# Kernel tuning notes

Measured on AMD Instinct MI355X. Metric: run time of the kernel, lower is better.

The kernel has to match this reference:

```python
import jax, jax.numpy as jnp
import numpy as np

EMBED_DIM = 768
NUM_HEADS = 12
HEAD_DIM = EMBED_DIM // NUM_HEADS


def setup_inputs() -> dict:
    key = jax.random.key(0)
    ks = jax.random.split(key, 9)
    B, N, D = 8, 1024, EMBED_DIM
    s = 1.0 / np.sqrt(D)
    x = jax.random.normal(ks[0], (B, N, D), dtype=jnp.float32)
    Wq = jax.random.normal(ks[1], (D, D), dtype=jnp.float32) * s
    bq = jnp.zeros((D,), dtype=jnp.float32)
    Wk = jax.random.normal(ks[2], (D, D), dtype=jnp.float32) * s
    bk = jnp.zeros((D,), dtype=jnp.float32)
    Wv = jax.random.normal(ks[3], (D, D), dtype=jnp.float32) * s
    bv = jnp.zeros((D,), dtype=jnp.float32)
    Wo = jax.random.normal(ks[4], (D, D), dtype=jnp.float32) * s
    bo = jnp.zeros((D,), dtype=jnp.float32)
    return {"x": x, "Wq": Wq, "bq": bq, "Wk": Wk, "bk": bk,
            "Wv": Wv, "bv": bv, "Wo": Wo, "bo": bo}


def reference(x, Wq, bq, Wk, bk, Wv, bv, Wo, bo):
    B, N, D = x.shape
    H, Hd = NUM_HEADS, HEAD_DIM
    # torch Linear: y = x @ W.T + b
    q = (x @ Wq.T + bq).reshape(B, N, H, Hd).transpose(0, 2, 1, 3)  # [B,H,N,Hd]
    k = (x @ Wk.T + bk).reshape(B, N, H, Hd).transpose(0, 2, 1, 3)
    v = (x @ Wv.T + bv).reshape(B, N, H, Hd).transpose(0, 2, 1, 3)
    # NOTE: original scales by embed_dim**-0.5 (not head_dim)
    scale = jnp.asarray(D, x.dtype) ** -0.5
    scores = jnp.einsum('bhnd,bhmd->bhnm', q, k) * scale  # [B,H,N,N]
    attn = jax.nn.softmax(scores, axis=-1)
    out = jnp.einsum('bhnm,bhmd->bhnd', attn, v)  # dropout: identity in eval
    out = out.transpose(0, 2, 1, 3).reshape(B, N, D)
    return out @ Wo.T + bo
```

## Files before the change

kernel.cpp:

```cpp
#include <hip/hip_runtime.h>
#include <math.h>


typedef __bf16 bf16x8 __attribute__((ext_vector_type(8)));
typedef float  f32x4  __attribute__((ext_vector_type(4)));
typedef unsigned u32x2 __attribute__((ext_vector_type(2)));
typedef unsigned u32x4 __attribute__((ext_vector_type(4)));
typedef unsigned short ushort_t;

__device__ __forceinline__ unsigned short f2bf(float f) {
    unsigned u = __float_as_uint(f);
    u += 0x7fffu + ((u >> 16) & 1u);
    return (unsigned short)(u >> 16);
}
__device__ __forceinline__ unsigned pk16(unsigned short lo, unsigned short hi) {
    return (unsigned)lo | ((unsigned)hi << 16);
}

#define GLL16(g, l)                                                                        \
    __builtin_amdgcn_global_load_lds((const __attribute__((address_space(1))) void*)(g),   \
                                     (__attribute__((address_space(3))) void*)(l), 16, 0, 0)

__global__ __launch_bounds__(256)
void cast_all(const float* __restrict__ x,
              const float* __restrict__ w0, const float* __restrict__ w1,
              const float* __restrict__ w2, const float* __restrict__ w3,
              ushort_t* __restrict__ xb, ushort_t* __restrict__ wb0,
              ushort_t* __restrict__ wb1, ushort_t* __restrict__ wb2,
              ushort_t* __restrict__ wb3)
{
    const int y = blockIdx.y;
    const float* s; ushort_t* d; int n;
    switch (y) {
        case 0:  s = x;  d = xb;  n = 8192 * 768; break;
        case 1:  s = w0; d = wb0; n = 768 * 768;  break;
        case 2:  s = w1; d = wb1; n = 768 * 768;  break;
        case 3:  s = w2; d = wb2; n = 768 * 768;  break;
        default: s = w3; d = wb3; n = 768 * 768;  break;
    }
    const int i = (blockIdx.x * 256 + threadIdx.x) * 8;
    if (i >= n) return;
    const float4 f0 = *(const float4*)(s + i);
    const float4 f1 = *(const float4*)(s + i + 4);
    ushort4 p0, p1;
    p0.x = f2bf(f0.x); p0.y = f2bf(f0.y); p0.z = f2bf(f0.z); p0.w = f2bf(f0.w);
    p1.x = f2bf(f1.x); p1.y = f2bf(f1.y); p1.z = f2bf(f1.z); p1.w = f2bf(f1.w);
    *(ushort4*)(d + i)     = p0;
    *(ushort4*)(d + i + 4) = p1;
}

__device__ __forceinline__ void gemm_core_mfma(
    const ushort_t* __restrict__ A, const ushort_t* __restrict__ W,
    int m0, int n0, ushort_t* smem, f32x4 acc[4][4])
{
    ushort_t* As = smem;
    ushort_t* Ws = smem + 4096;
    const int tid = threadIdx.x;
    const int L   = tid & 63;
    const int wv  = tid >> 6;
    const int wr  = wv >> 1, wc = wv & 1;
    const int c   = L & 15,  g  = L >> 4;

    const int c0 = tid, c1 = tid + 256;
    const int qs = ((tid & 3) ^ ((tid >> 3) & 3)) * 8;
    const ushort_t* a0 = A + (size_t)(m0 + (c0 >> 2)) * 768 + qs;
    const ushort_t* a1 = A + (size_t)(m0 + (c1 >> 2)) * 768 + qs;
    const ushort_t* w0 = W + (size_t)(n0 + (c0 >> 2)) * 768 + qs;
    const ushort_t* w1 = W + (size_t)(n0 + (c1 >> 2)) * 768 + qs;
    const int sg = (g ^ ((c >> 1) & 3)) * 8;

#pragma unroll
    for (int i = 0; i < 4; ++i)
#pragma unroll
        for (int j = 0; j < 4; ++j) acc[i][j] = (f32x4){0.f, 0.f, 0.f, 0.f};

    for (int k0 = 0; k0 < 768; k0 += 32) {
        __syncthreads();
        GLL16(a0 + k0, &As[(size_t)c0 * 8]);
        GLL16(a1 + k0, &As[(size_t)c1 * 8]);
        GLL16(w0 + k0, &Ws[(size_t)c0 * 8]);
        GLL16(w1 + k0, &Ws[(size_t)c1 * 8]);
        __syncthreads();
        bf16x8 af[4], bfr[4];
#pragma unroll
        for (int i = 0; i < 4; ++i)
            af[i] = *(const bf16x8*)&As[(wr * 64 + i * 16 + c) * 32 + sg];
#pragma unroll
        for (int j = 0; j < 4; ++j)
            bfr[j] = *(const bf16x8*)&Ws[(wc * 64 + j * 16 + c) * 32 + sg];
#pragma unroll
        for (int i = 0; i < 4; ++i)
#pragma unroll
            for (int j = 0; j < 4; ++j)
                acc[i][j] = __builtin_amdgcn_mfma_f32_16x16x32_bf16(
                    af[i], bfr[j], acc[i][j], 0, 0, 0);
    }
}

__global__ __launch_bounds__(256, 3)
void gemm_qkv(const ushort_t* __restrict__ xb,
              const ushort_t* __restrict__ wqb, const ushort_t* __restrict__ wkb,
              const ushort_t* __restrict__ wvb,
              const float* __restrict__ bq, const float* __restrict__ bk,
              const float* __restrict__ bv,
              ushort_t* __restrict__ Qh, ushort_t* __restrict__ Kl,
              ushort_t* __restrict__ Vl)
{
    __shared__ ushort_t smem[8192];
    const int z = blockIdx.z;
    const ushort_t* W   = (z == 0) ? wqb : (z == 1) ? wkb : wvb;
    const float*    bia = (z == 0) ? bq  : (z == 1) ? bk  : bv;
    const int m0 = blockIdx.y * 128, n0 = blockIdx.x * 128;
    f32x4 acc[4][4];
    gemm_core_mfma(xb, W, m0, n0, smem, acc);

    const int tid = threadIdx.x, L = tid & 63, wv2 = tid >> 6;
    const int wr = wv2 >> 1, wc = wv2 & 1, c = L & 15, g = L >> 4;
    ushort_t* scr = smem + wv2 * 1280;
    const int h = (n0 + wc * 64) >> 6;
    float bsv[4];
#pragma unroll
    for (int j = 0; j < 4; ++j) bsv[j] = bia[n0 + wc * 64 + j * 16 + c];

    __syncthreads();
#pragma unroll
    for (int i = 0; i < 4; ++i) {
        const int rowg = m0 + wr * 64 + i * 16;
        const int b  = rowg >> 10;
        const int nb = rowg & 1023;
        const int bh = b * 12 + h;
        if (z < 2) {
#pragma unroll
            for (int j = 0; j < 4; ++j)
#pragma unroll
                for (int r = 0; r < 4; ++r)
                    scr[(g * 4 + r) * 72 + j * 16 + c] = f2bf(acc[i][j][r] + bsv[j]);
            if (z == 0) {
                const int row = L >> 2, qp = L & 3;
                const u32x4 v0 = *(const u32x4*)&scr[row * 72 + qp * 16];
                const u32x4 v1 = *(const u32x4*)&scr[row * 72 + qp * 16 + 8];
                ushort_t* dst = Qh + ((size_t)bh * 1024 + nb + row) * 64 + qp * 16;
                *(u32x4*)dst       = v0;
                *(u32x4*)(dst + 8) = v1;
            } else {
                const int n16 = L >> 2, q1 = L & 3;
                const u32x4 va  = *(const u32x4*)&scr[n16 * 72 + q1 * 8];
                const u32x4 vb2 = *(const u32x4*)&scr[n16 * 72 + q1 * 8 + 32];
                ushort_t* base = Kl + (size_t)bh * 65536 + (size_t)(nb >> 4) * 1024;
                *(u32x4*)&base[q1 * 128 + n16 * 8]       = va;
                *(u32x4*)&base[512 + q1 * 128 + n16 * 8] = vb2;
            }
        } else {
#pragma unroll
            for (int j = 0; j < 4; ++j) {
                const unsigned w01 = pk16(f2bf(acc[i][j][0] + bsv[j]),
                                          f2bf(acc[i][j][1] + bsv[j]));
                const unsigned w23 = pk16(f2bf(acc[i][j][2] + bsv[j]),
                                          f2bf(acc[i][j][3] + bsv[j]));
                const int a = (j * 16 + c) * 20 + g * 4;
                *(unsigned*)&scr[a]     = w01;
                *(unsigned*)&scr[a + 2] = w23;
            }
            const u32x2 r0 = *(const u32x2*)&scr[L * 20];
            const u32x2 r1 = *(const u32x2*)&scr[L * 20 + 4];
            const u32x2 r2 = *(const u32x2*)&scr[L * 20 + 8];
            const u32x2 r3 = *(const u32x2*)&scr[L * 20 + 12];
            const int ht = L >> 4, cV = L & 15;
            const int T = nb >> 6, u = (nb >> 5) & 1, gVa = (nb >> 3) & 3;
            ushort_t* vb = Vl + (((size_t)(bh * 4 + ht) * 16 + T) * 2 + u) * 512 + cV * 8;
            *(u32x4*)&vb[gVa * 128]       = (u32x4){r0.x, r0.y, r1.x, r1.y};
            *(u32x4*)&vb[(gVa + 1) * 128] = (u32x4){r2.x, r2.y, r3.x, r3.y};
        }
    }
}

__global__ __launch_bounds__(256, 3)
void gemm_outp(const ushort_t* __restrict__ attnb, const ushort_t* __restrict__ wob,
               const float* __restrict__ bo, float* __restrict__ out)
{
    __shared__ ushort_t smem[8192];
    const int m0 = blockIdx.y * 128, n0 = blockIdx.x * 128;
    f32x4 acc[4][4];
    gemm_core_mfma(attnb, wob, m0, n0, smem, acc);
    const int tid = threadIdx.x, L = tid & 63, wv2 = tid >> 6;
    const int wr = wv2 >> 1, wc = wv2 & 1, c = L & 15, g = L >> 4;
#pragma unroll
    for (int i = 0; i < 4; ++i) {
        const int row = m0 + wr * 64 + i * 16 + g * 4;
#pragma unroll
        for (int j = 0; j < 4; ++j) {
            const int col = n0 + wc * 64 + j * 16 + c;
            const float bsvo = bo[col];
#pragma unroll
            for (int r = 0; r < 4; ++r)
                out[(size_t)(row + r) * 768 + col] = acc[i][j][r] + bsvo;
        }
    }
}

union FlashSmem {
    ushort_t ps[2][2][16 * 68];
    f32x4 comb[2][64 * 5];
};

__global__ __launch_bounds__(128, 3)
void flash_bf16(const ushort_t* __restrict__ Q, const ushort_t* __restrict__ Kl,
                const ushort_t* __restrict__ Vl, ushort_t* __restrict__ attnb)
{
    __shared__ FlashSmem sm;
    const int tid = threadIdx.x;
    const int wv = tid >> 6, L = tid & 63, c = L & 15, g = L >> 4;
    const int bh = blockIdx.y, q0 = blockIdx.x * 32;
    const float SC2 = 0.05205954985329743f;

    const ushort_t* Qp = Q + ((size_t)bh * 1024 + q0 + c) * 64 + g * 8;
    bf16x8 qf[2][2];
    qf[0][0] = *(const bf16x8*)Qp;
    qf[0][1] = *(const bf16x8*)(Qp + 32);
    qf[1][0] = *(const bf16x8*)(Qp + 1024);
    qf[1][1] = *(const bf16x8*)(Qp + 1056);

    const ushort_t* Kb = Kl + (size_t)bh * 65536 + (size_t)L * 8;
    const ushort_t* Vb = Vl + (size_t)bh * 65536 + (size_t)L * 8;

    f32x4 o[2][4];
#pragma unroll
    for (int w = 0; w < 2; ++w)
#pragma unroll
        for (int ht = 0; ht < 4; ++ht) o[w][ht] = (f32x4){0.f, 0.f, 0.f, 0.f};
    float ls[2] = {0.f, 0.f};

    const int Tbeg = wv * 8, Tend = Tbeg + 8;

    bf16x8 kf0[4], kf1[4];
#pragma unroll
    for (int ct = 0; ct < 4; ++ct) {
        const ushort_t* kp = Kb + (size_t)((Tbeg * 4 + ct) * 2) * 512;
        kf0[ct] = *(const bf16x8*)kp;
        kf1[ct] = *(const bf16x8*)(kp + 512);
    }

    for (int T = Tbeg; T < Tend; ++T) {
        bf16x8 vf0[4], vf1[4];
#pragma unroll
        for (int ht = 0; ht < 4; ++ht) {
            const ushort_t* vp = Vb + (size_t)((ht * 16 + T) * 2) * 512;
            vf0[ht] = *(const bf16x8*)vp;
            vf1[ht] = *(const bf16x8*)(vp + 512);
        }
        f32x4 s[2][4];
#pragma unroll
        for (int w = 0; w < 2; ++w)
#pragma unroll
            for (int ct = 0; ct < 4; ++ct) {
                f32x4 zz = (f32x4){0.f, 0.f, 0.f, 0.f};
                zz = __builtin_amdgcn_mfma_f32_16x16x32_bf16(kf0[ct], qf[w][0], zz, 0, 0, 0);
                zz = __builtin_amdgcn_mfma_f32_16x16x32_bf16(kf1[ct], qf[w][1], zz, 0, 0, 0);
                s[w][ct] = zz;
            }
        const int Tn = (T + 1 < Tend) ? T + 1 : T;
#pragma unroll
        for (int ct = 0; ct < 4; ++ct) {
            const ushort_t* kp = Kb + (size_t)((Tn * 4 + ct) * 2) * 512;
            kf0[ct] = *(const bf16x8*)kp;
            kf1[ct] = *(const bf16x8*)(kp + 512);
        }
#pragma unroll
        for (int w = 0; w < 2; ++w) {
#pragma unroll
            for (int ct = 0; ct < 4; ++ct) {
                float p[4];
#pragma unroll
                for (int r = 0; r < 4; ++r)
                    p[r] = __builtin_amdgcn_exp2f(s[w][ct][r] * SC2);
                ls[w] += (p[0] + p[1]) + (p[2] + p[3]);
                const unsigned w01 = __builtin_amdgcn_perm(
                    __float_as_uint(p[1]), __float_as_uint(p[0]), 0x07060302u);
                const unsigned w23 = __builtin_amdgcn_perm(
                    __float_as_uint(p[3]), __float_as_uint(p[2]), 0x07060302u);
                *(u32x2*)&sm.ps[wv][w][c * 68 + ct * 16 + g * 4] = (u32x2){w01, w23};
            }
        }
        const int pb = c * 68 + g * 8;
#pragma unroll
        for (int w = 0; w < 2; ++w) {
            const bf16x8 pf0 = __builtin_bit_cast(bf16x8, *(const u32x4*)&sm.ps[wv][w][pb]);
            const bf16x8 pf1 = __builtin_bit_cast(bf16x8, *(const u32x4*)&sm.ps[wv][w][pb + 32]);
#pragma unroll
            for (int ht = 0; ht < 4; ++ht) {
                o[w][ht] = __builtin_amdgcn_mfma_f32_16x16x32_bf16(vf0[ht], pf0, o[w][ht], 0, 0, 0);
                o[w][ht] = __builtin_amdgcn_mfma_f32_16x16x32_bf16(vf1[ht], pf1, o[w][ht], 0, 0, 0);
            }
        }
    }

    __syncthreads();

    const int other = wv ^ 1;
#pragma unroll
    for (int ht = 0; ht < 4; ++ht) sm.comb[other][L * 5 + ht] = o[other][ht];
    sm.comb[other][L * 5 + 4] = (f32x4){ls[other], 0.f, 0.f, 0.f};
    __syncthreads();

    f32x4 oc[4];
#pragma unroll
    for (int ht = 0; ht < 4; ++ht) oc[ht] = o[wv][ht] + sm.comb[wv][L * 5 + ht];
    float lc = ls[wv] + sm.comb[wv][L * 5 + 4].x;
    lc += __shfl_xor(lc, 16);
    lc += __shfl_xor(lc, 32);
    const float inv = 1.f / lc;

    ushort_t* strip = (ushort_t*)&sm.comb[wv][0];
#pragma unroll
    for (int ht = 0; ht < 4; ++ht) {
        const unsigned w0 = pk16(f2bf(oc[ht][0] * inv), f2bf(oc[ht][1] * inv));
        const unsigned w1 = pk16(f2bf(oc[ht][2] * inv), f2bf(oc[ht][3] * inv));
        *(u32x2*)&strip[c * 68 + ht * 16 + g * 4] = (u32x2){w0, w1};
    }
    const int b = bh / 12, h = bh % 12;
#pragma unroll
    for (int e = 0; e < 2; ++e) {
        const int row = e * 8 + (L >> 3);
        const int ch  = L & 7;
        const int si  = row * 68 + ch * 8;
        const u32x2 t0 = *(const u32x2*)&strip[si];
        const u32x2 t1 = *(const u32x2*)&strip[si + 4];
        *(u32x4*)&attnb[((size_t)(b * 1024 + q0 + wv * 16 + row)) * 768 + h * 64 + ch * 8]
            = (u32x4){t0.x, t0.y, t1.x, t1.y};
    }
}

extern "C" void kernel_launch(void* const* d_in, const int* in_sizes, int n_in,
                              void* d_out, int out_size, void* d_ws, size_t ws_size,
                              hipStream_t stream)
{
    const float* x  = (const float*)d_in[0];
    const float* Wq = (const float*)d_in[1];
    const float* bq = (const float*)d_in[2];
    const float* Wk = (const float*)d_in[3];
    const float* bk = (const float*)d_in[4];
    const float* Wv = (const float*)d_in[5];
    const float* bv = (const float*)d_in[6];
    const float* Wo = (const float*)d_in[7];
    const float* bo = (const float*)d_in[8];
    float* out = (float*)d_out;

    char* ws = (char*)d_ws;
    ushort_t* xb    = (ushort_t*)(ws);
    ushort_t* wqb   = (ushort_t*)(ws + 12582912);
    ushort_t* wkb   = (ushort_t*)(ws + 12582912 + 1179648);
    ushort_t* wvb   = (ushort_t*)(ws + 12582912 + 2359296);
    ushort_t* wob   = (ushort_t*)(ws + 12582912 + 3538944);
    ushort_t* Qh    = (ushort_t*)(ws + 17301504);
    ushort_t* Kl    = (ushort_t*)(ws + 29884416);
    ushort_t* Vl    = (ushort_t*)(ws + 42467328);
    ushort_t* attnb = (ushort_t*)(ws + 55050240);

    cast_all<<<dim3(3072, 5), 256, 0, stream>>>(x, Wq, Wk, Wv, Wo,
                                                xb, wqb, wkb, wvb, wob);
    gemm_qkv<<<dim3(6, 64, 3), 256, 0, stream>>>(xb, wqb, wkb, wvb,
                                                 bq, bk, bv, Qh, Kl, Vl);
    flash_bf16<<<dim3(32, 96), 128, 0, stream>>>(Qh, Kl, Vl, attnb);
    gemm_outp<<<dim3(6, 64), 256, 0, stream>>>(attnb, wob, bo, out);
}
```

Before: 222.3 us.

## Use single-wave flash blocks over full key range, drop cross-wave combine

The flash attention kernel now runs one 64-thread wave per block that walks all 16 key tiles, instead of two waves splitting keys in half and merging partial outputs through shared memory. This removes the two block barriers and the shared-memory combine step, and shrinks the shared-memory footprint. The grid is also transposed so consecutive blocks cover different batch-heads for the same query tile, which changes the cache locality of K/V reads. The cost is half the threads per block and twice the serial key loop length per wave, which may reduce latency hiding.

After: 198.7 us. 1.12x faster.

```diff
diff --git a/kernel.cpp b/kernel.cpp
--- a/kernel.cpp
+++ b/kernel.cpp
@@ -198,27 +198,22 @@
     }
 }
 
-union FlashSmem {
-    ushort_t ps[2][2][16 * 68];
-    f32x4 comb[2][64 * 5];
-};
-
-__global__ __launch_bounds__(128, 3)
+__global__ __launch_bounds__(64, 3)
 void flash_bf16(const ushort_t* __restrict__ Q, const ushort_t* __restrict__ Kl,
                 const ushort_t* __restrict__ Vl, ushort_t* __restrict__ attnb)
 {
-    __shared__ FlashSmem sm;
-    const int tid = threadIdx.x;
-    const int wv = tid >> 6, L = tid & 63, c = L & 15, g = L >> 4;
-    const int bh = blockIdx.y, q0 = blockIdx.x * 32;
+    __shared__ ushort_t Ps[2][16 * 68];
+    const int L = threadIdx.x;
+    const int c = L & 15, g = L >> 4;
+    const int bh = blockIdx.x, q0 = blockIdx.y * 32;
     const float SC2 = 0.05205954985329743f;
 
     const ushort_t* Qp = Q + ((size_t)bh * 1024 + q0 + c) * 64 + g * 8;
     bf16x8 qf[2][2];
     qf[0][0] = *(const bf16x8*)Qp;
     qf[0][1] = *(const bf16x8*)(Qp + 32);
-    qf[1][0] = *(const bf16x8*)(Qp + 1024);
-    qf[1][1] = *(const bf16x8*)(Qp + 1056);
+    qf[1][0] = *(const bf16x8*)(Qp + 16 * 64);
+    qf[1][1] = *(const bf16x8*)(Qp + 16 * 64 + 32);
 
     const ushort_t* Kb = Kl + (size_t)bh * 65536 + (size_t)L * 8;
     const ushort_t* Vb = Vl + (size_t)bh * 65536 + (size_t)L * 8;
@@ -230,17 +225,14 @@
         for (int ht = 0; ht < 4; ++ht) o[w][ht] = (f32x4){0.f, 0.f, 0.f, 0.f};
     float ls[2] = {0.f, 0.f};
 
-    const int Tbeg = wv * 8, Tend = Tbeg + 8;
-
     bf16x8 kf0[4], kf1[4];
 #pragma unroll
     for (int ct = 0; ct < 4; ++ct) {
-        const ushort_t* kp = Kb + (size_t)((Tbeg * 4 + ct) * 2) * 512;
-        kf0[ct] = *(const bf16x8*)kp;
-        kf1[ct] = *(const bf16x8*)(kp + 512);
-    }
-
-    for (int T = Tbeg; T < Tend; ++T) {
+        kf0[ct] = *(const bf16x8*)(Kb + (size_t)(ct * 2 + 0) * 512);
+        kf1[ct] = *(const bf16x8*)(Kb + (size_t)(ct * 2 + 1) * 512);
+    }
+
+    for (int T = 0; T < 16; ++T) {
         bf16x8 vf0[4], vf1[4];
 #pragma unroll
         for (int ht = 0; ht < 4; ++ht) {
@@ -258,7 +250,7 @@
                 zz = __builtin_amdgcn_mfma_f32_16x16x32_bf16(kf1[ct], qf[w][1], zz, 0, 0, 0);
                 s[w][ct] = zz;
             }
-        const int Tn = (T + 1 < Tend) ? T + 1 : T;
+        const int Tn = (T < 15) ? T + 1 : 15;
 #pragma unroll
         for (int ct = 0; ct < 4; ++ct) {
             const ushort_t* kp = Kb + (size_t)((Tn * 4 + ct) * 2) * 512;
@@ -278,14 +270,16 @@
                     __float_as_uint(p[1]), __float_as_uint(p[0]), 0x07060302u);
                 const unsigned w23 = __builtin_amdgcn_perm(
                     __float_as_uint(p[3]), __float_as_uint(p[2]), 0x07060302u);
-                *(u32x2*)&sm.ps[wv][w][c * 68 + ct * 16 + g * 4] = (u32x2){w01, w23};
-            }
-        }
-        const int pb = c * 68 + g * 8;
+                *(u32x2*)&Ps[w][c * 68 + ct * 16 + g * 4] = (u32x2){w01, w23};
+            }
+        }
 #pragma unroll
         for (int w = 0; w < 2; ++w) {
-            const bf16x8 pf0 = __builtin_bit_cast(bf16x8, *(const u32x4*)&sm.ps[wv][w][pb]);
-            const bf16x8 pf1 = __builtin_bit_cast(bf16x8, *(const u32x4*)&sm.ps[wv][w][pb + 32]);
+            const int pb = c * 68 + g * 8;
+            const u32x4 pa  = *(const u32x4*)&Ps[w][pb];
+            const u32x4 pbv = *(const u32x4*)&Ps[w][pb + 32];
+            const bf16x8 pf0 = __builtin_bit_cast(bf16x8, pa);
+            const bf16x8 pf1 = __builtin_bit_cast(bf16x8, pbv);
 #pragma unroll
             for (int ht = 0; ht < 4; ++ht) {
                 o[w][ht] = __builtin_amdgcn_mfma_f32_16x16x32_bf16(vf0[ht], pf0, o[w][ht], 0, 0, 0);
@@ -294,39 +288,29 @@
         }
     }
 
-    __syncthreads();
-
-    const int other = wv ^ 1;
-#pragma unroll
-    for (int ht = 0; ht < 4; ++ht) sm.comb[other][L * 5 + ht] = o[other][ht];
-    sm.comb[other][L * 5 + 4] = (f32x4){ls[other], 0.f, 0.f, 0.f};
-    __syncthreads();
-
-    f32x4 oc[4];
-#pragma unroll
-    for (int ht = 0; ht < 4; ++ht) oc[ht] = o[wv][ht] + sm.comb[wv][L * 5 + ht];
-    float lc = ls[wv] + sm.comb[wv][L * 5 + 4].x;
-    lc += __shfl_xor(lc, 16);
-    lc += __shfl_xor(lc, 32);
-    const float inv = 1.f / lc;
-
-    ushort_t* strip = (ushort_t*)&sm.comb[wv][0];
-#pragma unroll
-    for (int ht = 0; ht < 4; ++ht) {
-        const unsigned w0 = pk16(f2bf(oc[ht][0] * inv), f2bf(oc[ht][1] * inv));
-        const unsigned w1 = pk16(f2bf(oc[ht][2] * inv), f2bf(oc[ht][3] * inv));
-        *(u32x2*)&strip[c * 68 + ht * 16 + g * 4] = (u32x2){w0, w1};
-    }
     const int b = bh / 12, h = bh % 12;
 #pragma unroll
-    for (int e = 0; e < 2; ++e) {
-        const int row = e * 8 + (L >> 3);
-        const int ch  = L & 7;
-        const int si  = row * 68 + ch * 8;
-        const u32x2 t0 = *(const u32x2*)&strip[si];
-        const u32x2 t1 = *(const u32x2*)&strip[si + 4];
-        *(u32x4*)&attnb[((size_t)(b * 1024 + q0 + wv * 16 + row)) * 768 + h * 64 + ch * 8]
-            = (u32x4){t0.x, t0.y, t1.x, t1.y};
+    for (int w = 0; w < 2; ++w) {
+        float l = ls[w];
+        l += __shfl_xor(l, 16);
+        l += __shfl_xor(l, 32);
+        const float inv = 1.f / l;
+#pragma unroll
+        for (int ht = 0; ht < 4; ++ht) {
+            const unsigned w0 = pk16(f2bf(o[w][ht][0] * inv), f2bf(o[w][ht][1] * inv));
+            const unsigned w1 = pk16(f2bf(o[w][ht][2] * inv), f2bf(o[w][ht][3] * inv));
+            *(u32x2*)&Ps[w][c * 68 + ht * 16 + g * 4] = (u32x2){w0, w1};
+        }
+#pragma unroll
+        for (int e = 0; e < 2; ++e) {
+            const int row = e * 8 + (L >> 3);
+            const int ch  = L & 7;
+            const int si  = row * 68 + ch * 8;
+            const u32x2 t0 = *(const u32x2*)&Ps[w][si];
+            const u32x2 t1 = *(const u32x2*)&Ps[w][si + 4];
+            *(u32x4*)&attnb[((size_t)(b * 1024 + q0 + w * 16 + row)) * 768 + h * 64 + ch * 8]
+                = (u32x4){t0.x, t0.y, t1.x, t1.y};
+        }
     }
 }
 
@@ -360,6 +344,6 @@
                                                 xb, wqb, wkb, wvb, wob);
     gemm_qkv<<<dim3(6, 64, 3), 256, 0, stream>>>(xb, wqb, wkb, wvb,
                                                  bq, bk, bv, Qh, Kl, Vl);
-    flash_bf16<<<dim3(32, 96), 128, 0, stream>>>(Qh, Kl, Vl, attnb);
+    flash_bf16<<<dim3(96, 32), 64, 0, stream>>>(Qh, Kl, Vl, attnb);
     gemm_outp<<<dim3(6, 64), 256, 0, stream>>>(attnb, wob, bo, out);
 }
```
